# Optimization experiments

Hardware: AMD Instinct MI355X
Metric: run time of the kernel (lower is better)

The kernel has to match this reference:

```python
import jax, jax.numpy as jnp
import numpy as np

TOP_K = 256            # hard-coded top_k = min(max_k, 256) in the torch forward
N_CROSS = 1024         # n_cross_attention


def setup_inputs() -> dict:
    key = jax.random.key(0)
    k1, k2, k3, k4 = jax.random.split(key, 4)
    B, N, C, D = 8, 100000, 18, 128
    return {
        "centerness": jax.random.normal(k1, (B, N), dtype=jnp.float32),
        "cls_scores": jax.random.normal(k2, (B, N, C), dtype=jnp.float32),
        "points":     jax.random.normal(k3, (B, N, 3), dtype=jnp.float32),
        "features":   jax.random.normal(k4, (B, N, D), dtype=jnp.float32),
    }


def reference(centerness, cls_scores, points, features):
    # select_scores = cls.sigmoid() * centerness.sigmoid()[..., None]  -> [B, N, C]
    select_scores = jax.nn.sigmoid(cls_scores) * jax.nn.sigmoid(centerness)[..., None]
    max_scores = jnp.max(select_scores, axis=-1)  # [B, N]

    # cross-attention feature selection: topk(n_cross_attention) indices (cross_sampling=False branch)
    _, cross_inds = jax.lax.top_k(max_scores, N_CROSS)                       # [B, 1024]
    cross_features = jnp.take_along_axis(features, cross_inds[..., None], axis=1)  # [B, 1024, D]

    # stage-2 proposal selection: topk(256) then sort indices ascending
    _, inds = jax.lax.top_k(max_scores, TOP_K)    # [B, 256]
    sort_inds = jnp.sort(inds, axis=-1)           # [B, 256]
    feat_sel = jnp.take_along_axis(features, sort_inds[..., None], axis=1)   # [B, 256, D]
    pts_sel  = jnp.take_along_axis(points,   sort_inds[..., None], axis=1)   # [B, 256, 3]

    return pts_sel, feat_sel, sort_inds, cross_features
```

## Files before the change

### kernel.cpp

```cpp
#include <hip/hip_runtime.h>
#include <stdint.h>

#define BB 8
#define NN 100000
#define CC 18
#define DD 128
#define NCROSS 1024
#define TOPK 256
#define NBINS 8192
#define CCAP 4096
#define SEG 3125
#define RBLK 64

#define OFF_PTS 0
#define OFF_FEAT 6144
#define OFF_SI 268288
#define OFF_CROSS 270336

__device__ __forceinline__ float sigf(float x) {
  float e = (float)exp(-(double)x);
  return 1.0f / (1.0f + e);
}

__global__ void k_init(uint32_t* __restrict__ p, int n) {
  int i = blockIdx.x * 256 + threadIdx.x;
  if (i < n) p[i] = 0u;
}

__global__ void k_score(const float* __restrict__ cen, const float* __restrict__ cls,
                        uint32_t* __restrict__ keys, uint32_t* __restrict__ hist) {
  int b = blockIdx.y;
  int seg = blockIdx.x;
  __shared__ uint32_t h[NBINS];
  for (int j = threadIdx.x; j < NBINS; j += 256) h[j] = 0u;
  __syncthreads();
  int base = b * NN + seg * SEG;
  for (int it = threadIdx.x; it < SEG; it += 256) {
    int i = base + it;
    const float2* p2 = (const float2*)(cls + (size_t)i * CC);
    float m = -INFINITY;
#pragma unroll
    for (int c = 0; c < CC / 2; ++c) {
      float2 v = p2[c];
      m = fmaxf(m, fmaxf(v.x, v.y));
    }
    float s = sigf(m) * sigf(cen[i]);
    uint32_t k = __float_as_uint(s);
    keys[i] = k;
    atomicAdd(&h[k >> 19], 1u);
  }
  __syncthreads();
  for (int j = threadIdx.x; j < NBINS; j += 256) {
    uint32_t v = h[j];
    if (v) atomicAdd(&hist[b * NBINS + j], v);
  }
}

__global__ void k_select(const uint32_t* __restrict__ hist, uint32_t* __restrict__ cutoff) {
  int b = blockIdx.x;
  int t = threadIdx.x;
  __shared__ uint32_t h[NBINS];
  __shared__ uint32_t csum[256];
  for (int j = t; j < NBINS; j += 256) h[j] = hist[b * NBINS + j];
  __syncthreads();
  uint32_t s = 0;
  int base = t * 32;
#pragma unroll
  for (int j = 0; j < 32; ++j) s += h[base + ((j + t) & 31)];
  csum[t] = s;
  __syncthreads();
  for (int off = 1; off < 256; off <<= 1) {
    uint32_t v = csum[t];
    uint32_t a = (t + off < 256) ? csum[t + off] : 0u;
    __syncthreads();
    csum[t] = v + a;
    __syncthreads();
  }
  uint32_t St = csum[t];
  uint32_t St1 = (t < 255) ? csum[t + 1] : 0u;
  if (St >= NCROSS && St1 < NCROSS) {
    uint32_t acc = St1;
    int cb = base;
    for (int bin = base + 31; bin >= base; --bin) {
      acc += h[bin];
      if (acc >= NCROSS) { cb = bin; break; }
    }
    cutoff[b] = (uint32_t)cb;
  }
}

__global__ void k_compact(const uint32_t* __restrict__ keys, const uint32_t* __restrict__ cutoff,
                          uint32_t* __restrict__ cand_cnt, uint32_t* __restrict__ cand_key,
                          uint32_t* __restrict__ cand_idx) {
  int b = blockIdx.y;
  int n = blockIdx.x * 256 + threadIdx.x;
  bool pass = false;
  uint32_t k = 0;
  if (n < NN) {
    k = keys[b * NN + n];
    pass = (k >> 19) >= cutoff[b];
  }
  int lane = threadIdx.x & 63;
  unsigned long long mask = __ballot(pass);
  if (mask) {
    int leader = __ffsll(mask) - 1;
    uint32_t wbase = 0;
    if (lane == leader) wbase = atomicAdd(&cand_cnt[b], (uint32_t)__popcll(mask));
    wbase = __shfl(wbase, leader);
    if (pass) {
      uint32_t pos = wbase + (uint32_t)__popcll(mask & ((1ull << lane) - 1ull));
      if (pos < CCAP) {
        cand_key[b * CCAP + pos] = k;
        cand_idx[b * CCAP + pos] = (uint32_t)n;
      }
    }
  }
}

__global__ void k_rank2(const uint32_t* __restrict__ cand_cnt, const uint32_t* __restrict__ cand_key,
                        const uint32_t* __restrict__ cand_idx, uint32_t* __restrict__ ordered) {
  int b = blockIdx.y;
  uint32_t cnt = cand_cnt[b];
  if (cnt > CCAP) cnt = CCAP;
  uint32_t base = blockIdx.x * RBLK;
  if (base >= cnt) return;
  __shared__ uint64_t comp[CCAP];
  __shared__ uint32_t rsum[RBLK];
  int t = threadIdx.x;
  for (uint32_t j = t; j < cnt; j += 256) {
    comp[j] = ((uint64_t)cand_key[b * CCAP + j] << 32) | (uint32_t)(~cand_idx[b * CCAP + j]);
  }
  if (t < RBLK) rsum[t] = 0u;
  __syncthreads();
  uint32_t p = base + (t & 63);
  int part = t >> 6;
  if (p < cnt) {
    uint64_t mine = comp[p];
    uint32_t lo = (cnt * (uint32_t)part) >> 2;
    uint32_t hi = (cnt * (uint32_t)(part + 1)) >> 2;
    uint32_t r = 0;
    uint32_t j = lo;
    for (; j + 8 <= hi; j += 8) {
      uint64_t c0 = comp[j], c1 = comp[j + 1], c2 = comp[j + 2], c3 = comp[j + 3];
      uint64_t c4 = comp[j + 4], c5 = comp[j + 5], c6 = comp[j + 6], c7 = comp[j + 7];
      r += (c0 > mine) + (c1 > mine) + (c2 > mine) + (c3 > mine);
      r += (c4 > mine) + (c5 > mine) + (c6 > mine) + (c7 > mine);
    }
    for (; j < hi; ++j) r += (comp[j] > mine) ? 1u : 0u;
    atomicAdd(&rsum[t & 63], r);
  }
  __syncthreads();
  if (part == 0 && p < cnt) {
    uint32_t r = rsum[t & 63];
    if (r < NCROSS) ordered[b * NCROSS + r] = ~(uint32_t)comp[p];
  }
}

__global__ void k_sort256(const uint32_t* __restrict__ ordered, uint32_t* __restrict__ sel,
                          float* __restrict__ out_si) {
  int b = blockIdx.x;
  int t = threadIdx.x;
  __shared__ uint32_t idxs[TOPK];
  uint32_t v = ordered[b * NCROSS + t];
  idxs[t] = v;
  __syncthreads();
  int r = 0;
  for (int j = 0; j < TOPK; ++j) r += (idxs[j] < v) ? 1 : 0;
  sel[b * TOPK + r] = v;
  out_si[b * TOPK + r] = (float)v;
}

__global__ void k_gather(const float* __restrict__ features, const float* __restrict__ points,
                         const uint32_t* __restrict__ ordered, const uint32_t* __restrict__ sel,
                         float* __restrict__ out) {
  int g = blockIdx.x;
  int t = threadIdx.x;
  if (g < 1024) {
    int flat = g * 256 + t;
    int row = flat >> 5;
    int c4 = flat & 31;
    int b = row >> 10, j = row & 1023;
    uint32_t idx = ordered[b * NCROSS + j];
    const float4* src = (const float4*)(features + ((size_t)b * NN + idx) * DD);
    ((float4*)(out + OFF_CROSS))[flat] = src[c4];
  } else if (g < 1280) {
    int flat = (g - 1024) * 256 + t;
    int row = flat >> 5;
    int c4 = flat & 31;
    int b = row >> 8, j = row & 255;
    uint32_t idx = sel[b * TOPK + j];
    const float4* src = (const float4*)(features + ((size_t)b * NN + idx) * DD);
    ((float4*)(out + OFF_FEAT))[flat] = src[c4];
  } else {
    int b = g - 1280;
    uint32_t idx = sel[b * TOPK + t];
    const float* src = points + ((size_t)b * NN + idx) * 3;
    float* dst = out + OFF_PTS + ((size_t)b * TOPK + t) * 3;
    dst[0] = src[0];
    dst[1] = src[1];
    dst[2] = src[2];
  }
}

extern "C" void kernel_launch(void* const* d_in, const int* in_sizes, int n_in,
                              void* d_out, int out_size, void* d_ws, size_t ws_size,
                              hipStream_t stream) {
  const float* cen  = (const float*)d_in[0];
  const float* cls  = (const float*)d_in[1];
  const float* pts  = (const float*)d_in[2];
  const float* feat = (const float*)d_in[3];
  float* out = (float*)d_out;

  uint32_t* ws = (uint32_t*)d_ws;
  uint32_t* hist     = ws;
  uint32_t* cand_cnt = hist + BB * NBINS;
  uint32_t* cutoff   = cand_cnt + BB;
  uint32_t* cand_key = cutoff + BB;
  uint32_t* cand_idx = cand_key + BB * CCAP;
  uint32_t* ordered  = cand_idx + BB * CCAP;
  uint32_t* sel      = ordered + BB * NCROSS;
  uint32_t* keys     = sel + BB * TOPK;

  int nz = BB * NBINS + BB;
  k_init<<<(nz + 255) / 256, 256, 0, stream>>>(hist, nz);
  k_score<<<dim3(32, BB), 256, 0, stream>>>(cen, cls, keys, hist);
  k_select<<<BB, 256, 0, stream>>>(hist, cutoff);
  k_compact<<<dim3((NN + 255) / 256, BB), 256, 0, stream>>>(keys, cutoff, cand_cnt, cand_key, cand_idx);
  k_rank2<<<dim3(CCAP / RBLK, BB), 256, 0, stream>>>(cand_cnt, cand_key, cand_idx, ordered);
  k_sort256<<<BB, 256, 0, stream>>>(ordered, sel, out + OFF_SI);
  k_gather<<<1288, 256, 0, stream>>>(feat, pts, ordered, sel, out);
}
```

Measured before the change: 142.3 us.

## Stage class-score rows through shared memory with coalesced float4 loads and packed histogram

The scoring kernel now launches 1600 blocks of 500 rows instead of 256 blocks. Each block first loads its class-score tile into shared memory with coalesced float4 reads, so threads no longer do strided 72-byte per-row reads from global memory. The block histogram packs two 16-bit counters per 32-bit word, which halves shared-memory use and the per-block clear and flush cost. In exchange the kernel makes more global atomic flushes, and the tile plus histogram take about 52 KB of LDS per block, which limits occupancy.

```diff
diff --git a/kernel.cpp b/kernel.cpp
--- a/kernel.cpp
+++ b/kernel.cpp
@@ -9,8 +9,9 @@
 #define TOPK 256
 #define NBINS 8192
 #define CCAP 4096
-#define SEG 3125
 #define RBLK 64
+#define ROWS 500
+#define TILE4 2250
 
 #define OFF_PTS 0
 #define OFF_FEAT 6144
@@ -27,32 +28,39 @@
   if (i < n) p[i] = 0u;
 }
 
-__global__ void k_score(const float* __restrict__ cen, const float* __restrict__ cls,
-                        uint32_t* __restrict__ keys, uint32_t* __restrict__ hist) {
+__global__ void __launch_bounds__(256) k_score_v3(const float* __restrict__ cen,
+                                                  const float* __restrict__ cls,
+                                                  uint32_t* __restrict__ keys,
+                                                  uint32_t* __restrict__ hist) {
   int b = blockIdx.y;
-  int seg = blockIdx.x;
-  __shared__ uint32_t h[NBINS];
-  for (int j = threadIdx.x; j < NBINS; j += 256) h[j] = 0u;
-  __syncthreads();
-  int base = b * NN + seg * SEG;
-  for (int it = threadIdx.x; it < SEG; it += 256) {
-    int i = base + it;
-    const float2* p2 = (const float2*)(cls + (size_t)i * CC);
-    float m = -INFINITY;
+  int blk = blockIdx.x;
+  int t = threadIdx.x;
+  __shared__ float tile[ROWS * CC];
+  __shared__ uint32_t h[4096];
+  for (int i = t; i < 4096; i += 256) h[i] = 0u;
+  const float4* src = (const float4*)cls + ((size_t)b * 450000 + (size_t)blk * TILE4);
+  float4* dst = (float4*)tile;
+  for (int i = t; i < TILE4; i += 256) dst[i] = src[i];
+  __syncthreads();
+  int rowbase = blk * ROWS;
+  const float* cenb = cen + (size_t)b * NN + rowbase;
+  uint32_t* keyb = keys + (size_t)b * NN + rowbase;
+  for (int r = t; r < ROWS; r += 256) {
+    const float* p = tile + r * CC;
+    float m = p[0];
 #pragma unroll
-    for (int c = 0; c < CC / 2; ++c) {
-      float2 v = p2[c];
-      m = fmaxf(m, fmaxf(v.x, v.y));
-    }
-    float s = sigf(m) * sigf(cen[i]);
+    for (int c = 1; c < CC; ++c) m = fmaxf(m, p[c]);
+    float s = sigf(m) * sigf(cenb[r]);
     uint32_t k = __float_as_uint(s);
-    keys[i] = k;
-    atomicAdd(&h[k >> 19], 1u);
-  }
-  __syncthreads();
-  for (int j = threadIdx.x; j < NBINS; j += 256) {
-    uint32_t v = h[j];
-    if (v) atomicAdd(&hist[b * NBINS + j], v);
+    keyb[r] = k;
+    uint32_t bin = k >> 19;
+    atomicAdd(&h[bin & 4095], 1u << ((bin >> 12) << 4));
+  }
+  __syncthreads();
+  for (int i = t; i < 4096; i += 256) {
+    uint32_t v = h[i];
+    if (v & 0xffffu) atomicAdd(&hist[b * NBINS + i], v & 0xffffu);
+    if (v >> 16)     atomicAdd(&hist[b * NBINS + i + 4096], v >> 16);
   }
 }
 
@@ -223,7 +231,7 @@
 
   int nz = BB * NBINS + BB;
   k_init<<<(nz + 255) / 256, 256, 0, stream>>>(hist, nz);
-  k_score<<<dim3(32, BB), 256, 0, stream>>>(cen, cls, keys, hist);
+  k_score_v3<<<dim3(200, BB), 256, 0, stream>>>(cen, cls, keys, hist);
   k_select<<<BB, 256, 0, stream>>>(hist, cutoff);
   k_compact<<<dim3((NN + 255) / 256, BB), 256, 0, stream>>>(keys, cutoff, cand_cnt, cand_key, cand_idx);
   k_rank2<<<dim3(CCAP / RBLK, BB), 256, 0, stream>>>(cand_cnt, cand_key, cand_idx, ordered);
```

Result: slower. 152.7 us (+7.3%).
